# Kernel optimization log

Hardware: AMD Instinct MI355X
Metric: run time of the kernel (lower is better)

The kernel has to match this reference:

```python
import jax, jax.numpy as jnp
import numpy as np

NUM_HEADS = 8
WINDOW = 5
DILATION = 1


def _offsets(window, dilation):
    r = dilation * (window // 2)
    return [(dy, dx) for dy in range(-r, r + 1, dilation)
            for dx in range(-r, r + 1, dilation)]


def _neighbors(x, window, dilation):
    # x: [B, heads, head_dim, Hc, Wc] -> [B, heads, K, head_dim, Hc, Wc]
    B, Hn, hd, Hc, Wc = x.shape
    r = dilation * (window // 2)
    xp = jnp.pad(x, ((0, 0), (0, 0), (0, 0), (r, r), (r, r)))
    offs = _offsets(window, dilation)
    return jnp.stack(
        [xp[..., r + dy:r + dy + Hc, r + dx:r + dx + Wc] for dy, dx in offs],
        axis=2)


def _valid_mask(Hc, Wc, window, dilation):
    # [K, Hc, Wc] bool: True where the shifted neighbor lies inside the map
    ys = jnp.arange(Hc)
    xs = jnp.arange(Wc)
    offs = _offsets(window, dilation)
    return jnp.stack(
        [(((ys + dy) >= 0) & ((ys + dy) < Hc))[:, None]
         & (((xs + dx) >= 0) & ((xs + dx) < Wc))[None, :]
         for dy, dx in offs], axis=0)


def _align_to_query_grid(t, out_h, out_w, scale):
    # repeat coarse lattice onto the fine query grid via anchor indexing
    y = jnp.clip(jnp.arange(out_h) // scale, 0, t.shape[-2] - 1)
    x = jnp.clip(jnp.arange(out_w) // scale, 0, t.shape[-1] - 1)
    return jnp.take(jnp.take(t, y, axis=-2), x, axis=-1)


def setup_inputs() -> dict:
    key = jax.random.key(0)
    k1, k2 = jax.random.split(key)
    k = jax.random.normal(k1, (2, 128, 48, 48), dtype=jnp.float32)
    v = jax.random.normal(k2, (2, 128, 48, 48), dtype=jnp.float32)
    return {"k": k, "v": v, "query_height": 96, "query_width": 96,
            "scale_factor": 2}


def reference(k, v, query_height, query_width, scale_factor):
    B, C, Hc, Wc = k.shape
    hd = C // NUM_HEADS
    kh = k.reshape(B, NUM_HEADS, hd, Hc, Wc)
    vh = v.reshape(B, NUM_HEADS, hd, Hc, Wc)
    k_nb = _neighbors(kh, WINDOW, DILATION)  # [B,H,K,hd,Hc,Wc]
    v_nb = _neighbors(vh, WINDOW, DILATION)
    mask = _valid_mask(Hc, Wc, WINDOW, DILATION)  # [K,Hc,Wc]
    K = mask.shape[0]
    mask = jnp.broadcast_to(mask[None, None], (B, NUM_HEADS, K, Hc, Wc))
    k_nb = _align_to_query_grid(k_nb, query_height, query_width, scale_factor)
    v_nb = _align_to_query_grid(v_nb, query_height, query_width, scale_factor)
    mask = _align_to_query_grid(mask, query_height, query_width, scale_factor)
    return (k_nb, v_nb, mask)
```

## Files before the change

### kernel.cpp

```cpp
#include <hip/hip_runtime.h>


#define KV_F4    14745600
#define TOT_F4   30412800

typedef float f32x4 __attribute__((ext_vector_type(4)));

__global__ __launch_bounds__(256) void linear_sweep_kernel(
    const float* __restrict__ kp, const float* __restrict__ vp,
    float* __restrict__ out) {
    const int f = blockIdx.x * 256 + threadIdx.x;

    if (f < 2 * KV_F4) {
        const bool is_k = (f < KV_F4);
        const float* __restrict__ src = is_k ? kp : vp;
        const int f2 = is_k ? f : f - KV_F4;
        const int x4 = f2 % 24;  int t = f2 / 24;
        const int y  = t % 96;   t /= 96;
        const int d  = t % 16;   t /= 16;
        const int kk = t % 25;   t /= 25;
        const int kq = kk / 5;
        const int dy = kq - 2;
        const int dx = kk - kq * 5 - 2;

        const int yy  = (y >> 1) + dy;
        const bool vy = (unsigned)yy < 48u;
        const int xc0 = 2 * x4 + dx;
        const int xc1 = xc0 + 1;
        const bool v0 = vy && ((unsigned)xc0 < 48u);
        const bool v1 = vy && ((unsigned)xc1 < 48u);

        const int yc = vy ? yy : 0;
        const int x0 = min(max(xc0, 0), 47);
        const int x1 = min(max(xc1, 0), 47);

        const int base = ((t * 16 + d) * 48 + yc) * 48;
        float a0 = src[base + x0];
        float a1 = src[base + x1];
        a0 = v0 ? a0 : 0.0f;
        a1 = v1 ? a1 : 0.0f;
        f32x4 o4 = {a0, a0, a1, a1};
        __builtin_nontemporal_store(o4, reinterpret_cast<f32x4*>(out) + f);
    } else {
        const int f2 = f - 2 * KV_F4;
        const int x4 = f2 % 24;  int t = f2 / 24;
        const int y  = t % 96;   t /= 96;
        const int kk = t % 25;
        const int kq = kk / 5;
        const int dy = kq - 2;
        const int dx = kk - kq * 5 - 2;

        const int yy  = (y >> 1) + dy;
        const bool vy = (unsigned)yy < 48u;
        const int xc0 = 2 * x4 + dx;
        const bool v0 = vy && ((unsigned)xc0 < 48u);
        const bool v1 = vy && ((unsigned)(xc0 + 1) < 48u);

        const float m0 = v0 ? 1.0f : 0.0f;
        const float m1 = v1 ? 1.0f : 0.0f;
        f32x4 o4 = {m0, m0, m1, m1};
        __builtin_nontemporal_store(o4, reinterpret_cast<f32x4*>(out) + f);
    }
}

extern "C" void kernel_launch(void* const* d_in, const int* in_sizes, int n_in,
                              void* d_out, int out_size, void* d_ws, size_t ws_size,
                              hipStream_t stream) {
    const float* k = (const float*)d_in[0];
    const float* v = (const float*)d_in[1];
    float* out = (float*)d_out;

    linear_sweep_kernel<<<118800, 256, 0, stream>>>(k, v, out);
}
```

Before: 488.0 us.

## Stage each k/v channel plane in LDS and expand all window offsets per block

```diff
diff --git a/kernel.cpp b/kernel.cpp
--- a/kernel.cpp
+++ b/kernel.cpp
@@ -1,65 +1,82 @@
 #include <hip/hip_runtime.h>
 
 
-#define KV_F4    14745600
-#define TOT_F4   30412800
+#define KV_ELEMS  58982400LL
+#define MASK_OFF  117964800LL
 
 typedef float f32x4 __attribute__((ext_vector_type(4)));
 
-__global__ __launch_bounds__(256) void linear_sweep_kernel(
+__global__ __launch_bounds__(256) void expand_lds_kernel(
     const float* __restrict__ kp, const float* __restrict__ vp,
-    float* __restrict__ out) {
-    const int f = blockIdx.x * 256 + threadIdx.x;
+    float* __restrict__ out_k, float* __restrict__ out_v,
+    float* __restrict__ out_m) {
+    const int bid = blockIdx.x;
+    const int tid = threadIdx.x;
 
-    if (f < 2 * KV_F4) {
-        const bool is_k = (f < KV_F4);
+    __shared__ float S[2304];
+
+    if (bid < 512) {
+        const bool is_k = bid < 256;
+        const int p = is_k ? bid : bid - 256;
+        const int z = p >> 4;
+        const int d = p & 15;
         const float* __restrict__ src = is_k ? kp : vp;
-        const int f2 = is_k ? f : f - KV_F4;
-        const int x4 = f2 % 24;  int t = f2 / 24;
-        const int y  = t % 96;   t /= 96;
-        const int d  = t % 16;   t /= 16;
-        const int kk = t % 25;   t /= 25;
-        const int kq = kk / 5;
-        const int dy = kq - 2;
-        const int dx = kk - kq * 5 - 2;
+        float* __restrict__ dst = is_k ? out_k : out_v;
 
-        const int yy  = (y >> 1) + dy;
-        const bool vy = (unsigned)yy < 48u;
-        const int xc0 = 2 * x4 + dx;
-        const int xc1 = xc0 + 1;
-        const bool v0 = vy && ((unsigned)xc0 < 48u);
-        const bool v1 = vy && ((unsigned)xc1 < 48u);
+        const f32x4* sp = reinterpret_cast<const f32x4*>(src) + p * 576;
+        f32x4* Sf4 = reinterpret_cast<f32x4*>(S);
+        Sf4[tid]       = sp[tid];
+        Sf4[tid + 256] = sp[tid + 256];
+        if (tid < 64) Sf4[tid + 512] = sp[tid + 512];
+        __syncthreads();
 
-        const int yc = vy ? yy : 0;
-        const int x0 = min(max(xc0, 0), 47);
-        const int x1 = min(max(xc1, 0), 47);
+        f32x4* dstf4 = reinterpret_cast<f32x4*>(dst);
+        const int obase = (z * 25 * 16 + d) * 2304;
 
-        const int base = ((t * 16 + d) * 48 + yc) * 48;
-        float a0 = src[base + x0];
-        float a1 = src[base + x1];
-        a0 = v0 ? a0 : 0.0f;
-        a1 = v1 ? a1 : 0.0f;
-        f32x4 o4 = {a0, a0, a1, a1};
-        __builtin_nontemporal_store(o4, reinterpret_cast<f32x4*>(out) + f);
+        for (int kk = 0; kk < 25; ++kk) {
+            const int kq = kk / 5;
+            const int dy = kq - 2;
+            const int dx = kk - kq * 5 - 2;
+            const int ob = obase + kk * (16 * 2304);
+#pragma unroll
+            for (int j = 0; j < 9; ++j) {
+                const int idx = j * 256 + tid;
+                const int y   = idx / 24;
+                const int x4  = idx - y * 24;
+                const int yy  = (y >> 1) + dy;
+                const bool vy = (unsigned)yy < 48u;
+                const int xc0 = 2 * x4 + dx;
+                const bool v0 = vy && ((unsigned)xc0 < 48u);
+                const bool v1 = vy && ((unsigned)(xc0 + 1) < 48u);
+                const int rb = (vy ? yy : 0) * 48;
+                float a0 = S[rb + min(max(xc0, 0), 47)];
+                float a1 = S[rb + min(max(xc0 + 1, 0), 47)];
+                a0 = v0 ? a0 : 0.0f;
+                a1 = v1 ? a1 : 0.0f;
+                dstf4[ob + idx] = (f32x4){a0, a0, a1, a1};
+            }
+        }
     } else {
-        const int f2 = f - 2 * KV_F4;
-        const int x4 = f2 % 24;  int t = f2 / 24;
-        const int y  = t % 96;   t /= 96;
-        const int kk = t % 25;
-        const int kq = kk / 5;
-        const int dy = kq - 2;
-        const int dx = kk - kq * 5 - 2;
-
-        const int yy  = (y >> 1) + dy;
-        const bool vy = (unsigned)yy < 48u;
-        const int xc0 = 2 * x4 + dx;
-        const bool v0 = vy && ((unsigned)xc0 < 48u);
-        const bool v1 = vy && ((unsigned)(xc0 + 1) < 48u);
-
-        const float m0 = v0 ? 1.0f : 0.0f;
-        const float m1 = v1 ? 1.0f : 0.0f;
-        f32x4 o4 = {m0, m0, m1, m1};
-        __builtin_nontemporal_store(o4, reinterpret_cast<f32x4*>(out) + f);
+        const int mb = bid - 512;
+        int f = mb * 2048 + tid;
+        f32x4* mo = reinterpret_cast<f32x4*>(out_m);
+#pragma unroll
+        for (int j = 0; j < 8; ++j, f += 256) {
+            const int x4 = f % 24;  int t = f / 24;
+            const int y  = t % 96;  t /= 96;
+            const int kk = t % 25;
+            const int kq = kk / 5;
+            const int dy = kq - 2;
+            const int dx = kk - kq * 5 - 2;
+            const int yy  = (y >> 1) + dy;
+            const bool vy = (unsigned)yy < 48u;
+            const int xc0 = 2 * x4 + dx;
+            const bool v0 = vy && ((unsigned)xc0 < 48u);
+            const bool v1 = vy && ((unsigned)(xc0 + 1) < 48u);
+            const float m0 = v0 ? 1.0f : 0.0f;
+            const float m1 = v1 ? 1.0f : 0.0f;
+            mo[f] = (f32x4){m0, m0, m1, m1};
+        }
     }
 }
 
@@ -69,6 +86,9 @@
     const float* k = (const float*)d_in[0];
     const float* v = (const float*)d_in[1];
     float* out = (float*)d_out;
+    float* out_k = out;
+    float* out_v = out + KV_ELEMS;
+    float* out_m = out + MASK_OFF;
 
-    linear_sweep_kernel<<<118800, 256, 0, stream>>>(k, v, out);
+    expand_lds_kernel<<<962, 256, 0, stream>>>(k, v, out_k, out_v, out_m);
 }
```

Measured after the change: 486.5 us. Within noise of the previous version (-0.3%).
